# Kernel optimization log

Hardware: AMD Instinct MI355X
Metric: run time of the kernel (lower is better)

## Reference

```python
import jax, jax.numpy as jnp
import numpy as np

N_NODES = 50000
N_EDGES = 800000
D = 128


def setup_inputs() -> dict:
    key = jax.random.key(0)
    ks = jax.random.split(key, 8)
    # xavier-uniform bound for [D, D]
    bound = np.sqrt(6.0 / (D + D)).astype(np.float32)
    x = jax.random.normal(ks[0], (N_NODES, D), dtype=jnp.float32)
    edge_index = jax.random.randint(ks[1], (2, N_EDGES), 0, N_NODES)
    W0 = jax.random.uniform(ks[2], (D, D), jnp.float32, -bound, bound)
    W1 = jax.random.uniform(ks[3], (D, D), jnp.float32, -bound, bound)
    W2 = jax.random.uniform(ks[4], (D, D), jnp.float32, -bound, bound)
    b0 = jnp.zeros((D,), jnp.float32)
    b1 = jnp.zeros((D,), jnp.float32)
    b2 = jnp.zeros((D,), jnp.float32)
    return {"x": x, "edge_index": edge_index,
            "W0": W0, "b0": b0, "W1": W1, "b1": b1, "W2": W2, "b2": b2}


def _gcn_conv(h, W, b, row, col, norm, n):
    # PyG GCNConv: x' = hat(D)^-1/2 hat(A) hat(D)^-1/2 (h W) + b
    hw = h @ W                                   # [N, D]
    msg = norm[:, None] * hw[row]                # gather from source nodes
    agg = jax.ops.segment_sum(msg, col, num_segments=n)  # scatter-add to targets
    return agg + b


def reference(x, edge_index, W0, b0, W1, b1, W2, b2):
    n = x.shape[0]
    loops = jnp.arange(n)
    # add self-loops (PyG GCNConv default)
    row = jnp.concatenate([edge_index[0], loops])
    col = jnp.concatenate([edge_index[1], loops])
    deg = jax.ops.segment_sum(jnp.ones(row.shape, x.dtype), col, num_segments=n)
    dinv = jnp.where(deg > 0, jax.lax.rsqrt(deg), 0.0)
    norm = dinv[row] * dinv[col]
    # dropout omitted (eval/inference mode)
    res = []
    h = x
    for W, b in ((W0, b0), (W1, b1), (W2, b2)):
        h = jnp.tanh(_gcn_conv(h, W, b, row, col, norm, n))
        res.append(h)
    return jnp.stack(res, axis=1)  # [N, n_layers, D]
```

## Files before the change

kernel.cpp:

```cpp
#include <hip/hip_runtime.h>
#include <math.h>

#define N_NODES 50000
#define N_EDGES 800000
#define D 128
#define NPAD 50048
#define NBLK 196

typedef unsigned int uint32;
typedef __attribute__((ext_vector_type(8))) short short8;
typedef __attribute__((ext_vector_type(4))) float f32x4;

__device__ __forceinline__ ushort f2bf(float f) {
    uint32 u = __float_as_uint(f);
    u = (u + 0x7fff + ((u >> 16) & 1)) >> 16;
    return (ushort)u;
}
__device__ __forceinline__ float bf2f(ushort u) {
    return __uint_as_float(((uint32)u) << 16);
}


__global__ __launch_bounds__(256) void k_count(const int* __restrict__ col,
                                               int* __restrict__ counts,
                                               int* __restrict__ rank_buf) {
    int i4 = (blockIdx.x * 256 + threadIdx.x) * 4;
    if (i4 < N_EDGES) {
        int4 c = *(const int4*)(col + i4);
        int4 r;
        r.x = atomicAdd(&counts[c.x], 1);
        r.y = atomicAdd(&counts[c.y], 1);
        r.z = atomicAdd(&counts[c.z], 1);
        r.w = atomicAdd(&counts[c.w], 1);
        *(int4*)(rank_buf + i4) = r;
    }
}

__global__ __launch_bounds__(256) void k_scan_local(const int* __restrict__ counts,
                                                    int* __restrict__ offsets,
                                                    int* __restrict__ partials) {
    __shared__ int wsum[4];
    int tid = threadIdx.x;
    int i = blockIdx.x * 256 + tid;
    int v = (i < N_NODES) ? counts[i] : 0;
    int lane = tid & 63, wv = tid >> 6;
    int x = v;
    #pragma unroll
    for (int off = 1; off < 64; off <<= 1) {
        int y = __shfl_up(x, off);
        if (lane >= off) x += y;
    }
    if (lane == 63) wsum[wv] = x;
    __syncthreads();
    int b0 = wsum[0], b1 = wsum[1], b2 = wsum[2], b3 = wsum[3];
    int base = (wv > 0 ? b0 : 0) + (wv > 1 ? b1 : 0) + (wv > 2 ? b2 : 0);
    if (i < N_NODES) offsets[i] = base + x - v;
    if (tid == 255) partials[blockIdx.x] = b0 + b1 + b2 + b3;
}

__global__ __launch_bounds__(256) void k_scan_add(int* __restrict__ offsets,
                                                  const int* __restrict__ partials,
                                                  const int* __restrict__ counts,
                                                  float* __restrict__ dinv) {
    __shared__ int wsum[4];
    int tid = threadIdx.x;
    int p = (tid < (int)blockIdx.x && tid < NBLK) ? partials[tid] : 0;
    int lane = tid & 63, wv = tid >> 6;
    #pragma unroll
    for (int off = 32; off; off >>= 1) p += __shfl_down(p, off);
    if (lane == 0) wsum[wv] = p;
    __syncthreads();
    int base = wsum[0] + wsum[1] + wsum[2] + wsum[3];
    int i = blockIdx.x * 256 + tid;
    if (i < N_NODES) {
        offsets[i] += base;
        dinv[i] = rsqrtf((float)counts[i] + 1.0f);
    }
    if (i == 0) offsets[N_NODES] = N_EDGES;
}

__global__ __launch_bounds__(256) void k_fill(const int* __restrict__ row,
                                              const int* __restrict__ col,
                                              const int* __restrict__ offsets,
                                              const int* __restrict__ rank_buf,
                                              int* __restrict__ csr_rows) {
    int i4 = (blockIdx.x * 256 + threadIdx.x) * 4;
    if (i4 < N_EDGES) {
        int4 c = *(const int4*)(col + i4);
        int4 r = *(const int4*)(rank_buf + i4);
        int4 rw = *(const int4*)(row + i4);
        csr_rows[offsets[c.x] + r.x] = rw.x;
        csr_rows[offsets[c.y] + r.y] = rw.y;
        csr_rows[offsets[c.z] + r.z] = rw.z;
        csr_rows[offsets[c.w] + r.w] = rw.w;
    }
}

__global__ __launch_bounds__(256) void k_wconv(const float* __restrict__ W0,
                                               const float* __restrict__ W1,
                                               const float* __restrict__ W2,
                                               ushort* __restrict__ wt) {
    int i = blockIdx.x * 256 + threadIdx.x;
    int l = i >> 14;
    int flat = i & 16383;
    int n = flat >> 7, k = flat & 127;
    const float* W = (l == 0) ? W0 : (l == 1) ? W1 : W2;
    wt[i] = f2bf(W[k * 128 + n]);
}

#define BM 64
#define LDA 136
#define NTILES ((N_NODES + BM - 1) / BM)

__global__ __launch_bounds__(256) void k_gemm(const float* __restrict__ hf,
                                              const ushort* __restrict__ hb,
                                              const ushort* __restrict__ wt,
                                              const float* __restrict__ dinv,
                                              ushort* __restrict__ hw) {
    __shared__ __align__(16) ushort Wt[D * LDA];
    __shared__ __align__(16) ushort As[BM * LDA];
    int tid = threadIdx.x;
    int lane = tid & 63;
    int w = tid >> 6;
    int quad = lane >> 4;
    int m16 = lane & 15;

    #pragma unroll
    for (int i = 0; i < 8; ++i) {
        int chunk = i * 256 + tid;
        int n = chunk >> 4, k16 = chunk & 15;
        *(short8*)(Wt + n * LDA + k16 * 8) = *(const short8*)(wt + n * 128 + k16 * 8);
    }
    __syncthreads();

    int row0 = blockIdx.x * BM;
    int arow = row0 + w * 16 + m16;

    f32x4 acc[8];
    #pragma unroll
    for (int ct = 0; ct < 8; ++ct) acc[ct] = (f32x4){0.f, 0.f, 0.f, 0.f};

    #pragma unroll
    for (int ks = 0; ks < 4; ++ks) {
        short8 a;
        if (hf) {
            if (arow < N_NODES) {
                const float4* p = (const float4*)(hf + (size_t)arow * D + ks * 32 + quad * 8);
                float4 x0 = p[0], x1 = p[1];
                a[0] = (short)f2bf(x0.x); a[1] = (short)f2bf(x0.y);
                a[2] = (short)f2bf(x0.z); a[3] = (short)f2bf(x0.w);
                a[4] = (short)f2bf(x1.x); a[5] = (short)f2bf(x1.y);
                a[6] = (short)f2bf(x1.z); a[7] = (short)f2bf(x1.w);
            } else {
                a = (short8){};
            }
        } else {
            a = *(const short8*)(hb + (size_t)arow * D + ks * 32 + quad * 8);
        }
        #pragma unroll
        for (int ct = 0; ct < 8; ++ct) {
            short8 b = *(const short8*)(Wt + (ct * 16 + m16) * LDA + ks * 32 + quad * 8);
            acc[ct] = __builtin_amdgcn_mfma_f32_16x16x32_bf16(a, b, acc[ct], 0, 0, 0);
        }
    }

    float dv[4];
    #pragma unroll
    for (int r = 0; r < 4; ++r) {
        int row = row0 + w * 16 + quad * 4 + r;
        dv[r] = (row < N_NODES) ? dinv[row] : 0.f;
    }
    #pragma unroll
    for (int ct = 0; ct < 8; ++ct) {
        #pragma unroll
        for (int r = 0; r < 4; ++r)
            As[(w * 16 + quad * 4 + r) * LDA + ct * 16 + m16] = f2bf(acc[ct][r] * dv[r]);
    }
    #pragma unroll
    for (int i = 0; i < 4; ++i) {
        int chunk = i * 64 + lane;
        int r = chunk >> 4, c8 = chunk & 15;
        int row = row0 + w * 16 + r;
        if (row < N_NODES) {
            short8 v = *(const short8*)(As + (w * 16 + r) * LDA + c8 * 8);
            *(short8*)(hw + (size_t)row * D + c8 * 8) = v;
        }
    }
}

__global__ __launch_bounds__(256) void k_agg(const ushort* __restrict__ hw,
                                             const float* __restrict__ dinv,
                                             const int* __restrict__ offsets,
                                             const int* __restrict__ csr_rows,
                                             const float* __restrict__ bias,
                                             float* __restrict__ out, int layer,
                                             ushort* __restrict__ hnext, int write_next) {
    int node = blockIdx.x * 4 + (threadIdx.x >> 6);
    int lane = threadIdx.x & 63;
    int q = lane >> 4;
    int m = lane & 15;

    float acc[8] = {};
    int s = offsets[node], e = offsets[node + 1];
    int j = s + q;
    for (; j + 4 < e; j += 8) {
        int r0 = csr_rows[j];
        int r1 = csr_rows[j + 4];
        short8 v0 = *((const short8*)(hw + (size_t)r0 * D) + m);
        short8 v1 = *((const short8*)(hw + (size_t)r1 * D) + m);
        #pragma unroll
        for (int i = 0; i < 8; ++i)
            acc[i] += bf2f((ushort)v0[i]) + bf2f((ushort)v1[i]);
    }
    for (; j < e; j += 4) {
        int r = csr_rows[j];
        short8 v = *((const short8*)(hw + (size_t)r * D) + m);
        #pragma unroll
        for (int i = 0; i < 8; ++i) acc[i] += bf2f((ushort)v[i]);
    }
    #pragma unroll
    for (int i = 0; i < 8; ++i) {
        acc[i] += __shfl_xor(acc[i], 16);
        acc[i] += __shfl_xor(acc[i], 32);
    }

    if (q == 0) {
        float di = dinv[node];
        short8 sv = *((const short8*)(hw + (size_t)node * D) + m);
        float4 ba = ((const float4*)bias)[2 * m];
        float4 bb = ((const float4*)bias)[2 * m + 1];
        float bv[8] = {ba.x, ba.y, ba.z, ba.w, bb.x, bb.y, bb.z, bb.w};
        float o[8];
        #pragma unroll
        for (int i = 0; i < 8; ++i)
            o[i] = tanhf(di * (acc[i] + bf2f((ushort)sv[i])) + bv[i]);
        float* op = out + ((size_t)node * 3 + layer) * D;
        ((float4*)op)[2 * m]     = make_float4(o[0], o[1], o[2], o[3]);
        ((float4*)op)[2 * m + 1] = make_float4(o[4], o[5], o[6], o[7]);
        if (write_next) {
            short8 nv;
            #pragma unroll
            for (int i = 0; i < 8; ++i) nv[i] = (short)f2bf(o[i]);
            *((short8*)(hnext + (size_t)node * D) + m) = nv;
        }
    }
}


extern "C" void kernel_launch(void* const* d_in, const int* in_sizes, int n_in,
                              void* d_out, int out_size, void* d_ws, size_t ws_size,
                              hipStream_t stream) {
    const float* x  = (const float*)d_in[0];
    const int*   ei = (const int*)d_in[1];
    const float* W0 = (const float*)d_in[2];
    const float* b0 = (const float*)d_in[3];
    const float* W1 = (const float*)d_in[4];
    const float* b1 = (const float*)d_in[5];
    const float* W2 = (const float*)d_in[6];
    const float* b2 = (const float*)d_in[7];
    float* out = (float*)d_out;

    const int* row = ei;
    const int* col = ei + N_EDGES;

    float*  dinv    = (float*)d_ws;
    int*    counts  = (int*)(dinv + NPAD);
    int*    offsets = counts + NPAD;
    int*    partials= offsets + NPAD;
    ushort* wt      = (ushort*)(partials + 256);
    int*    rank_buf= (int*)(wt + 3 * 16384);
    int*    csr     = rank_buf + N_EDGES;
    ushort* hw      = (ushort*)(csr + N_EDGES);
    ushort* hnext   = hw + (size_t)NPAD * D;

    int nb_e4 = (N_EDGES / 4 + 255) / 256;

    hipMemsetAsync(counts, 0, NPAD * sizeof(int), stream);
    k_wconv<<<192, 256, 0, stream>>>(W0, W1, W2, wt);
    k_count<<<nb_e4, 256, 0, stream>>>(col, counts, rank_buf);
    k_scan_local<<<NBLK, 256, 0, stream>>>(counts, offsets, partials);
    k_scan_add<<<NBLK, 256, 0, stream>>>(offsets, partials, counts, dinv);
    k_fill<<<nb_e4, 256, 0, stream>>>(row, col, offsets, rank_buf, csr);

    int nb_agg = N_NODES / 4;

    const float* bs_[3] = {b0, b1, b2};
    for (int l = 0; l < 3; ++l) {
        if (l == 0) k_gemm<<<NTILES, 256, 0, stream>>>(x, (const ushort*)nullptr, wt, dinv, hw);
        else        k_gemm<<<NTILES, 256, 0, stream>>>((const float*)nullptr, hnext, wt + l * 16384, dinv, hw);
        k_agg<<<nb_agg, 256, 0, stream>>>(hw, dinv, offsets, csr, bs_[l], out, l,
                                          hnext, l < 2 ? 1 : 0);
    }
}
```

Measured before the change: 312.7 us.

## Fuse count with weight conversion, drop bf16 hnext, stage A tile in LDS

Merges the weight-conversion and degree-count kernels into a single launch, and doubles the edges handled per thread in count and fill. The aggregation kernel no longer writes a bf16 copy of the next-layer input. The GEMM instead reads the previous layer's fp32 output directly from the strided output tensor, converts it to bf16 and stages the A tile in LDS with coalesced loads. This removes one launch and a write stream per layer, at the cost of reading fp32 instead of bf16 for layers 1 and 2 and adding extra LDS traffic.

```diff
diff --git a/kernel.cpp b/kernel.cpp
--- a/kernel.cpp
+++ b/kernel.cpp
@@ -20,21 +20,43 @@
     return __uint_as_float(((uint32)u) << 16);
 }
 
-
-__global__ __launch_bounds__(256) void k_count(const int* __restrict__ col,
-                                               int* __restrict__ counts,
-                                               int* __restrict__ rank_buf) {
-    int i4 = (blockIdx.x * 256 + threadIdx.x) * 4;
-    if (i4 < N_EDGES) {
-        int4 c = *(const int4*)(col + i4);
-        int4 r;
-        r.x = atomicAdd(&counts[c.x], 1);
-        r.y = atomicAdd(&counts[c.y], 1);
-        r.z = atomicAdd(&counts[c.z], 1);
-        r.w = atomicAdd(&counts[c.w], 1);
-        *(int4*)(rank_buf + i4) = r;
-    }
-}
+#define WCONV_BLKS 192
+
+__global__ __launch_bounds__(256) void k_count_wconv(const int* __restrict__ col,
+                                                     int* __restrict__ counts,
+                                                     int* __restrict__ rank_buf,
+                                                     const float* __restrict__ W0,
+                                                     const float* __restrict__ W1,
+                                                     const float* __restrict__ W2,
+                                                     ushort* __restrict__ wt) {
+    int tid = threadIdx.x;
+    if (blockIdx.x < WCONV_BLKS) {
+        int i = blockIdx.x * 256 + tid;
+        int l = i >> 14;
+        int flat = i & 16383;
+        int n = flat >> 7, k = flat & 127;
+        const float* W = (l == 0) ? W0 : (l == 1) ? W1 : W2;
+        wt[i] = f2bf(W[k * 128 + n]);
+    } else {
+        int i8 = ((blockIdx.x - WCONV_BLKS) * 256 + tid) * 8;
+        if (i8 < N_EDGES) {
+            int4 c0 = *(const int4*)(col + i8);
+            int4 c1 = *(const int4*)(col + i8 + 4);
+            int4 r0, r1;
+            r0.x = atomicAdd(&counts[c0.x], 1);
+            r0.y = atomicAdd(&counts[c0.y], 1);
+            r0.z = atomicAdd(&counts[c0.z], 1);
+            r0.w = atomicAdd(&counts[c0.w], 1);
+            r1.x = atomicAdd(&counts[c1.x], 1);
+            r1.y = atomicAdd(&counts[c1.y], 1);
+            r1.z = atomicAdd(&counts[c1.z], 1);
+            r1.w = atomicAdd(&counts[c1.w], 1);
+            *(int4*)(rank_buf + i8)     = r0;
+            *(int4*)(rank_buf + i8 + 4) = r1;
+        }
+    }
+}
+
 
 __global__ __launch_bounds__(256) void k_scan_local(const int* __restrict__ counts,
                                                     int* __restrict__ offsets,
@@ -84,36 +106,30 @@
                                               const int* __restrict__ offsets,
                                               const int* __restrict__ rank_buf,
                                               int* __restrict__ csr_rows) {
-    int i4 = (blockIdx.x * 256 + threadIdx.x) * 4;
-    if (i4 < N_EDGES) {
-        int4 c = *(const int4*)(col + i4);
-        int4 r = *(const int4*)(rank_buf + i4);
-        int4 rw = *(const int4*)(row + i4);
-        csr_rows[offsets[c.x] + r.x] = rw.x;
-        csr_rows[offsets[c.y] + r.y] = rw.y;
-        csr_rows[offsets[c.z] + r.z] = rw.z;
-        csr_rows[offsets[c.w] + r.w] = rw.w;
-    }
-}
-
-__global__ __launch_bounds__(256) void k_wconv(const float* __restrict__ W0,
-                                               const float* __restrict__ W1,
-                                               const float* __restrict__ W2,
-                                               ushort* __restrict__ wt) {
-    int i = blockIdx.x * 256 + threadIdx.x;
-    int l = i >> 14;
-    int flat = i & 16383;
-    int n = flat >> 7, k = flat & 127;
-    const float* W = (l == 0) ? W0 : (l == 1) ? W1 : W2;
-    wt[i] = f2bf(W[k * 128 + n]);
+    int i8 = (blockIdx.x * 256 + threadIdx.x) * 8;
+    if (i8 < N_EDGES) {
+        int4 c0 = *(const int4*)(col + i8);
+        int4 c1 = *(const int4*)(col + i8 + 4);
+        int4 r0 = *(const int4*)(rank_buf + i8);
+        int4 r1 = *(const int4*)(rank_buf + i8 + 4);
+        int4 w0 = *(const int4*)(row + i8);
+        int4 w1 = *(const int4*)(row + i8 + 4);
+        csr_rows[offsets[c0.x] + r0.x] = w0.x;
+        csr_rows[offsets[c0.y] + r0.y] = w0.y;
+        csr_rows[offsets[c0.z] + r0.z] = w0.z;
+        csr_rows[offsets[c0.w] + r0.w] = w0.w;
+        csr_rows[offsets[c1.x] + r1.x] = w1.x;
+        csr_rows[offsets[c1.y] + r1.y] = w1.y;
+        csr_rows[offsets[c1.z] + r1.z] = w1.z;
+        csr_rows[offsets[c1.w] + r1.w] = w1.w;
+    }
 }
 
 #define BM 64
 #define LDA 136
 #define NTILES ((N_NODES + BM - 1) / BM)
 
-__global__ __launch_bounds__(256) void k_gemm(const float* __restrict__ hf,
-                                              const ushort* __restrict__ hb,
+__global__ __launch_bounds__(256) void k_gemm(const float* __restrict__ h, int hstride,
                                               const ushort* __restrict__ wt,
                                               const float* __restrict__ dinv,
                                               ushort* __restrict__ hw) {
@@ -124,6 +140,7 @@
     int w = tid >> 6;
     int quad = lane >> 4;
     int m16 = lane & 15;
+    int row0 = blockIdx.x * BM;
 
     #pragma unroll
     for (int i = 0; i < 8; ++i) {
@@ -131,32 +148,27 @@
         int n = chunk >> 4, k16 = chunk & 15;
         *(short8*)(Wt + n * LDA + k16 * 8) = *(const short8*)(wt + n * 128 + k16 * 8);
     }
+    #pragma unroll
+    for (int p = 0; p < 8; ++p) {
+        int flat = p * 256 + tid;
+        int r = flat >> 5, c4 = flat & 31;
+        int row = row0 + r;
+        ushort4 u = {0, 0, 0, 0};
+        if (row < N_NODES) {
+            float4 v = *(const float4*)(h + (size_t)row * hstride + c4 * 4);
+            u.x = f2bf(v.x); u.y = f2bf(v.y); u.z = f2bf(v.z); u.w = f2bf(v.w);
+        }
+        *(ushort4*)(As + r * LDA + c4 * 4) = u;
+    }
     __syncthreads();
 
-    int row0 = blockIdx.x * BM;
-    int arow = row0 + w * 16 + m16;
-
     f32x4 acc[8];
     #pragma unroll
     for (int ct = 0; ct < 8; ++ct) acc[ct] = (f32x4){0.f, 0.f, 0.f, 0.f};
 
     #pragma unroll
     for (int ks = 0; ks < 4; ++ks) {
-        short8 a;
-        if (hf) {
-            if (arow < N_NODES) {
-                const float4* p = (const float4*)(hf + (size_t)arow * D + ks * 32 + quad * 8);
-                float4 x0 = p[0], x1 = p[1];
-                a[0] = (short)f2bf(x0.x); a[1] = (short)f2bf(x0.y);
-                a[2] = (short)f2bf(x0.z); a[3] = (short)f2bf(x0.w);
-                a[4] = (short)f2bf(x1.x); a[5] = (short)f2bf(x1.y);
-                a[6] = (short)f2bf(x1.z); a[7] = (short)f2bf(x1.w);
-            } else {
-                a = (short8){};
-            }
-        } else {
-            a = *(const short8*)(hb + (size_t)arow * D + ks * 32 + quad * 8);
-        }
+        short8 a = *(const short8*)(As + (w * 16 + m16) * LDA + ks * 32 + quad * 8);
         #pragma unroll
         for (int ct = 0; ct < 8; ++ct) {
             short8 b = *(const short8*)(Wt + (ct * 16 + m16) * LDA + ks * 32 + quad * 8);
@@ -193,8 +205,7 @@
                                              const int* __restrict__ offsets,
                                              const int* __restrict__ csr_rows,
                                              const float* __restrict__ bias,
-                                             float* __restrict__ out, int layer,
-                                             ushort* __restrict__ hnext, int write_next) {
+                                             float* __restrict__ out, int layer) {
     int node = blockIdx.x * 4 + (threadIdx.x >> 6);
     int lane = threadIdx.x & 63;
     int q = lane >> 4;
@@ -237,12 +248,6 @@
         float* op = out + ((size_t)node * 3 + layer) * D;
         ((float4*)op)[2 * m]     = make_float4(o[0], o[1], o[2], o[3]);
         ((float4*)op)[2 * m + 1] = make_float4(o[4], o[5], o[6], o[7]);
-        if (write_next) {
-            short8 nv;
-            #pragma unroll
-            for (int i = 0; i < 8; ++i) nv[i] = (short)f2bf(o[i]);
-            *((short8*)(hnext + (size_t)node * D) + m) = nv;
-        }
     }
 }
 
@@ -271,24 +276,23 @@
     int*    rank_buf= (int*)(wt + 3 * 16384);
     int*    csr     = rank_buf + N_EDGES;
     ushort* hw      = (ushort*)(csr + N_EDGES);
-    ushort* hnext   = hw + (size_t)NPAD * D;
-
-    int nb_e4 = (N_EDGES / 4 + 255) / 256;
+
+    int nb_e8 = (N_EDGES / 8 + 255) / 256;
 
     hipMemsetAsync(counts, 0, NPAD * sizeof(int), stream);
-    k_wconv<<<192, 256, 0, stream>>>(W0, W1, W2, wt);
-    k_count<<<nb_e4, 256, 0, stream>>>(col, counts, rank_buf);
+    k_count_wconv<<<WCONV_BLKS + nb_e8, 256, 0, stream>>>(col, counts, rank_buf,
+                                                          W0, W1, W2, wt);
     k_scan_local<<<NBLK, 256, 0, stream>>>(counts, offsets, partials);
     k_scan_add<<<NBLK, 256, 0, stream>>>(offsets, partials, counts, dinv);
-    k_fill<<<nb_e4, 256, 0, stream>>>(row, col, offsets, rank_buf, csr);
+    k_fill<<<nb_e8, 256, 0, stream>>>(row, col, offsets, rank_buf, csr);
 
     int nb_agg = N_NODES / 4;
 
     const float* bs_[3] = {b0, b1, b2};
     for (int l = 0; l < 3; ++l) {
-        if (l == 0) k_gemm<<<NTILES, 256, 0, stream>>>(x, (const ushort*)nullptr, wt, dinv, hw);
-        else        k_gemm<<<NTILES, 256, 0, stream>>>((const float*)nullptr, hnext, wt + l * 16384, dinv, hw);
-        k_agg<<<nb_agg, 256, 0, stream>>>(hw, dinv, offsets, csr, bs_[l], out, l,
-                                          hnext, l < 2 ? 1 : 0);
-    }
-}
+        const float* h = (l == 0) ? x : (out + (size_t)(l - 1) * D);
+        int stride = (l == 0) ? D : 3 * D;
+        k_gemm<<<NTILES, 256, 0, stream>>>(h, stride, wt + l * 16384, dinv, hw);
+        k_agg<<<nb_agg, 256, 0, stream>>>(hw, dinv, offsets, csr, bs_[l], out, l);
+    }
+}
```

Result: no change. 306.6 us (-1.9%).
